# Kernel tuning notes

Hardware: AMD Instinct MI355X
Metric: run time of the kernel (lower is better)

## Reference

```python
import jax, jax.numpy as jnp
import numpy as np

N_NODES = 100000
N_EDGES = 1600000
D_FEAT = 128
HIDDEN = 128
HEADS = 4
OUT_C = HIDDEN // HEADS  # 32
N_CLASSES = 10
N_GRAPHS = 64
NEG_SLOPE = 0.2


def glorot(key, shape, fan_in, fan_out):
    s = jnp.sqrt(6.0 / (fan_in + fan_out))
    return jax.random.uniform(key, shape, minval=-s, maxval=s, dtype=jnp.float32)


def setup_inputs() -> dict:
    key = jax.random.key(0)
    ks = jax.random.split(key, 24)
    x = jax.random.normal(ks[0], (N_NODES, D_FEAT), dtype=jnp.float32)
    src = jax.random.randint(ks[1], (N_EDGES,), 0, N_NODES, dtype=jnp.int32)
    off = jax.random.randint(ks[2], (N_EDGES,), 1, N_NODES, dtype=jnp.int32)
    dst = ((src + off) % N_NODES).astype(jnp.int32)  # guarantees no self-loops
    edge_index = jnp.stack([src, dst], axis=0)
    batch = jnp.sort(jax.random.randint(ks[3], (N_NODES,), 0, N_GRAPHS, dtype=jnp.int32))
    inp = {"x": x, "edge_index": edge_index, "batch": batch}
    # GATConv layer params: W [in, H*C] (lin_l == lin_r), att_l/att_r [H, C], bias [H*C]
    ins = [D_FEAT, HIDDEN, HIDDEN]
    for i in range(3):
        k = 4 + 4 * i
        inp[f"W{i+1}"] = glorot(ks[k], (ins[i], HEADS * OUT_C), ins[i], HEADS * OUT_C)
        inp[f"al{i+1}"] = glorot(ks[k + 1], (HEADS, OUT_C), HEADS * OUT_C, 1)
        inp[f"ar{i+1}"] = glorot(ks[k + 2], (HEADS, OUT_C), HEADS * OUT_C, 1)
        inp[f"b{i+1}"] = jnp.zeros((HEADS * OUT_C,), jnp.float32)
    inp["lin1_w"] = glorot(ks[16], (HIDDEN, HIDDEN), HIDDEN, HIDDEN)
    inp["lin1_b"] = jnp.zeros((HIDDEN,), jnp.float32)
    inp["lin2_w"] = glorot(ks[17], (HIDDEN, N_CLASSES), HIDDEN, N_CLASSES)
    inp["lin2_b"] = jnp.zeros((N_CLASSES,), jnp.float32)
    return inp


def gat_layer(x, src, dst, W, att_l, att_r, bias):
    n = x.shape[0]
    H, C = att_l.shape
    xw = (x @ W).reshape(n, H, C)                       # Theta x
    al = jnp.einsum('nhc,hc->nh', xw, att_l)
    ar = jnp.einsum('nhc,hc->nh', xw, att_r)
    loop = jnp.arange(n, dtype=src.dtype)
    s = jnp.concatenate([src, loop])                    # add self-loops
    d = jnp.concatenate([dst, loop])
    logits = jax.nn.leaky_relu(al[s] + ar[d], NEG_SLOPE)  # [E+N, H]
    m = jax.ops.segment_max(logits, d, num_segments=n)    # segment softmax over dst
    e = jnp.exp(logits - m[d])
    z = jax.ops.segment_sum(e, d, num_segments=n)
    alpha = e / z[d]
    msg = xw[s] * alpha[:, :, None]                     # [E+N, H, C]
    out = jax.ops.segment_sum(msg, d, num_segments=n)   # scatter-add aggregate
    return out.reshape(n, H * C) + bias


def reference(x, edge_index, batch,
              W1, al1, ar1, b1, W2, al2, ar2, b2, W3, al3, ar3, b3,
              lin1_w, lin1_b, lin2_w, lin2_b):
    src, dst = edge_index[0], edge_index[1]
    h = jax.nn.relu(gat_layer(x, src, dst, W1, al1, ar1, b1))
    h = jax.nn.relu(gat_layer(h, src, dst, W2, al2, ar2, b2))
    h = jax.nn.relu(gat_layer(h, src, dst, W3, al3, ar3, b3))
    last = h
    # global mean pool over graphs in the batch
    s = jax.ops.segment_sum(h, batch, num_segments=N_GRAPHS)
    cnt = jax.ops.segment_sum(jnp.ones((h.shape[0],), h.dtype), batch, num_segments=N_GRAPHS)
    pooled = s / jnp.maximum(cnt, 1.0)[:, None]
    g = jax.nn.relu(pooled @ lin1_w + lin1_b)           # dropout inactive (eval)
    logits = g @ lin2_w + lin2_b
    return (jax.nn.log_softmax(logits, axis=-1), last)
```

## Files before the change

### kernel.cpp

```cpp
#include <hip/hip_runtime.h>
#include <math.h>


#define LRELU(x) ((x) > 0.f ? (x) : 0.2f*(x))
#define SH 8
#define TILE 4096
#define EPT 16
#define PSL 64

typedef __attribute__((ext_vector_type(8))) short s16x8;
typedef __attribute__((ext_vector_type(4))) float f32x4;

__device__ inline unsigned short f2bf(float f){
  unsigned u = __float_as_uint(f);
  u += 0x7fff + ((u >> 16) & 1);
  return (unsigned short)(u >> 16);
}

__global__ void k_init(int* __restrict__ bcnt, float* __restrict__ psum,
                       const float* __restrict__ W0, const float* __restrict__ W1,
                       const float* __restrict__ W2, unsigned short* __restrict__ wt3){
  int t = threadIdx.x;
  if (blockIdx.x == 0){
    bcnt[t] = 0; bcnt[256 + t] = 0;
    for (int i = t; i < 8192; i += 256) psum[i] = 0.f;
    return;
  }
  int e = ((int)blockIdx.x - 1)*256 + t;
  int layer = e >> 14, rem = e & 16383;
  int k = rem >> 7, nn = rem & 127;
  const float* Ws = layer == 0 ? W0 : (layer == 1 ? W1 : W2);
  wt3[layer*16384 + nn*128 + k] = f2bf(Ws[k*128 + nn]);
}

template<bool BF16IN>
__device__ __forceinline__ void gemm_body(
    unsigned short* Xl, unsigned short* Cl,
    const void* __restrict__ Xv, const unsigned short* __restrict__ Wtg,
    const float* __restrict__ attl, const float* __restrict__ attr,
    unsigned short* __restrict__ XW, float* __restrict__ AL, float* __restrict__ AR,
    int n, int bid, int gstride)
{
  int t = threadIdx.x;
  int lane = t & 63, w = t >> 6;
  int l15 = lane & 15, quad = lane >> 4;
  int ntiles = (n + 63) >> 6;
  int r_ = t >> 2, seg = t & 3;
  const unsigned short* Bp0 = Wtg + (w*32 + l15)*128 + quad*8;
  const unsigned short* Bp1 = Bp0 + 16*128;
  s16x8 b0r[4], b1r[4];
  #pragma unroll
  for (int ks = 0; ks < 4; ks++){
    b0r[ks] = *(const s16x8*)(Bp0 + ks*32);
    b1r[ks] = *(const s16x8*)(Bp1 + ks*32);
  }
  for (int tile = bid; tile < ntiles; tile += gstride){
    int row0 = tile << 6;
    {
      int grow = row0 + r_;
      unsigned short* dp = &Xl[r_*136 + seg*32];
      if (grow < n){
        if (BF16IN){
          const uint4* gp = (const uint4*)((const unsigned short*)Xv + (size_t)grow*128 + seg*32);
          #pragma unroll
          for (int i = 0; i < 4; i++) ((uint4*)dp)[i] = gp[i];
        } else {
          const float4* gp = (const float4*)((const float*)Xv + (size_t)grow*128 + seg*32);
          #pragma unroll
          for (int i = 0; i < 8; i++){
            float4 v = gp[i];
            ((unsigned*)dp)[i*2]   = (unsigned)f2bf(v.x) | ((unsigned)f2bf(v.y) << 16);
            ((unsigned*)dp)[i*2+1] = (unsigned)f2bf(v.z) | ((unsigned)f2bf(v.w) << 16);
          }
        }
      } else {
        #pragma unroll
        for (int i = 0; i < 4; i++) ((uint4*)dp)[i] = make_uint4(0,0,0,0);
      }
    }
    __syncthreads();
    f32x4 acc[4][2];
    #pragma unroll
    for (int rt = 0; rt < 4; rt++){ acc[rt][0] = (f32x4){0,0,0,0}; acc[rt][1] = (f32x4){0,0,0,0}; }
    #pragma unroll
    for (int ks = 0; ks < 4; ks++){
      #pragma unroll
      for (int rt = 0; rt < 4; rt++){
        s16x8 a = *(const s16x8*)&Xl[(rt*16 + l15)*136 + ks*32 + quad*8];
        acc[rt][0] = __builtin_amdgcn_mfma_f32_16x16x32_bf16(a, b0r[ks], acc[rt][0], 0, 0, 0);
        acc[rt][1] = __builtin_amdgcn_mfma_f32_16x16x32_bf16(a, b1r[ks], acc[rt][1], 0, 0, 0);
      }
    }
    #pragma unroll
    for (int rt = 0; rt < 4; rt++)
      #pragma unroll
      for (int c2 = 0; c2 < 2; c2++)
        #pragma unroll
        for (int r = 0; r < 4; r++)
          Cl[(rt*16 + quad*4 + r)*136 + w*32 + c2*16 + l15] = f2bf(acc[rt][c2][r]);
    __syncthreads();
    {
      int grow = row0 + r_;
      if (grow < n){
        const unsigned short* sp = &Cl[r_*136 + seg*32];
        uint4 uu[4];
        #pragma unroll
        for (int i = 0; i < 4; i++) uu[i] = ((const uint4*)sp)[i];
        unsigned short* gx = XW + (size_t)grow*128 + seg*32;
        #pragma unroll
        for (int i = 0; i < 4; i++) ((uint4*)gx)[i] = uu[i];
        const unsigned* up = (const unsigned*)uu;
        const float4* alp = (const float4*)(attl + seg*32);
        const float4* arp = (const float4*)(attr + seg*32);
        float pl = 0.f, pr = 0.f;
        #pragma unroll
        for (int i = 0; i < 8; i++){
          unsigned ua = up[i*2], ub = up[i*2+1];
          float x0 = __uint_as_float(ua << 16);
          float x1 = __uint_as_float(ua & 0xffff0000u);
          float x2 = __uint_as_float(ub << 16);
          float x3 = __uint_as_float(ub & 0xffff0000u);
          float4 av = alp[i];
          float4 rv = arp[i];
          pl += x0*av.x + x1*av.y + x2*av.z + x3*av.w;
          pr += x0*rv.x + x1*rv.y + x2*rv.z + x3*rv.w;
        }
        AL[grow*4 + seg] = pl;
        AR[grow*4 + seg] = pr;
      }
    }
  }
}

template<bool BF16IN>
__global__ __launch_bounds__(256) void k_gemm(
    const void* __restrict__ Xv, const unsigned short* __restrict__ Wtg,
    const float* __restrict__ attl, const float* __restrict__ attr,
    unsigned short* __restrict__ XW, float* __restrict__ AL, float* __restrict__ AR, int n)
{
  __shared__ unsigned short Xl[64*136];
  __shared__ unsigned short Cl[64*136];
  gemm_body<BF16IN>(Xl, Cl, Xv, Wtg, attl, attr, XW, AL, AR, n, blockIdx.x, gridDim.x);
}

__global__ __launch_bounds__(256) void k_fuse1(
    const int* __restrict__ dst, int* __restrict__ bcnt, int E, int nparts,
    const float* __restrict__ X, const unsigned short* __restrict__ Wtg,
    const float* __restrict__ attl, const float* __restrict__ attr,
    unsigned short* __restrict__ XW, float* __restrict__ AL, float* __restrict__ AR, int n)
{
  __shared__ unsigned short Xl[64*136];
  __shared__ unsigned short Cl[64*136];
  if ((int)blockIdx.x < nparts){
    int* lh = (int*)Xl;
    int t = threadIdx.x;
    for (int j = t; j < 512; j += 256) lh[j] = 0;
    __syncthreads();
    int base = blockIdx.x * TILE;
    int lim = min(base + TILE, E);
    for (int e = base + t; e < lim; e += 256)
      atomicAdd(&lh[dst[e] >> SH], 1);
    __syncthreads();
    for (int j = t; j < 512; j += 256){
      int v = lh[j];
      if (v) atomicAdd(&bcnt[j], v);
    }
    return;
  }
  gemm_body<false>(Xl, Cl, X, Wtg, attl, attr, XW, AL, AR, n,
                   (int)blockIdx.x - nparts, (int)gridDim.x - nparts);
}

__global__ __launch_bounds__(256) void k_bscan(const int* __restrict__ bcnt,
    int* __restrict__ bstart, int* __restrict__ bfill, int NB, int E,
    const int* __restrict__ batch, int* __restrict__ gstart, int n){
  int t = threadIdx.x;
  if (blockIdx.x == 1){
    int g = t;
    if (g > 64) return;
    int lo = 0, hi = n;
    while (lo < hi){
      int mid = (lo + hi) >> 1;
      if (batch[mid] < g) lo = mid + 1; else hi = mid;
    }
    gstart[g] = lo;
    return;
  }
  __shared__ int c[512];
  __shared__ int ps[256];
  for (int j = t; j < 512; j += 256) c[j] = (j < NB) ? bcnt[j] : 0;
  __syncthreads();
  int b0 = 2*t;
  int v0 = c[b0], v1 = c[b0+1];
  int ts = v0 + v1;
  ps[t] = ts; __syncthreads();
  for (int off = 1; off < 256; off <<= 1){
    int x = (t >= off) ? ps[t-off] : 0; __syncthreads();
    ps[t] += x; __syncthreads();
  }
  int pre = ps[t] - ts;
  if (b0   < NB){ bstart[b0]   = pre;    bfill[b0]   = pre; }
  if (b0+1 < NB){ bstart[b0+1] = pre+v0; bfill[b0+1] = pre+v0; }
  if (t == 0) bstart[NB] = E;
}

__global__ __launch_bounds__(256) void k_part(const int* __restrict__ src,
    const int* __restrict__ dst, int* __restrict__ bfill,
    int2* __restrict__ tmp, int E){
  __shared__ int2 reorder[TILE];
  __shared__ int lhist[512], lscan[512], lgbase[512];
  __shared__ int ps[256];
  int t = threadIdx.x;
  int tb = blockIdx.x * TILE;
  int tilecnt = min(TILE, E - tb);
  for (int j = t; j < 512; j += 256) lhist[j] = 0;
  __syncthreads();
  int ss[EPT], dd[EPT], rk[EPT];
  #pragma unroll
  for (int i = 0; i < EPT; i++){
    int e = tb + t + i*256;
    if (e < E){
      ss[i] = src[e]; dd[i] = dst[e];
      rk[i] = atomicAdd(&lhist[dd[i] >> SH], 1);
    }
  }
  __syncthreads();
  int b0 = 2*t;
  int v0 = lhist[b0], v1 = lhist[b0+1];
  int ts = v0 + v1;
  ps[t] = ts; __syncthreads();
  for (int off = 1; off < 256; off <<= 1){
    int x = (t >= off) ? ps[t-off] : 0; __syncthreads();
    ps[t] += x; __syncthreads();
  }
  int pre = ps[t] - ts;
  int ex0 = pre, ex1 = pre + v0;
  lscan[b0] = ex0; lscan[b0+1] = ex1;
  if (v0 > 0){ int gb = atomicAdd(&bfill[b0],   v0); lgbase[b0]   = gb - ex0; }
  if (v1 > 0){ int gb = atomicAdd(&bfill[b0+1], v1); lgbase[b0+1] = gb - ex1; }
  __syncthreads();
  #pragma unroll
  for (int i = 0; i < EPT; i++){
    int e = tb + t + i*256;
    if (e < E){
      int b = dd[i] >> SH;
      reorder[lscan[b] + rk[i]] = make_int2(ss[i], dd[i]);
    }
  }
  __syncthreads();
  for (int j = t; j < tilecnt; j += 256){
    int2 p = reorder[j];
    tmp[lgbase[p.y >> SH] + j] = p;
  }
}

__global__ __launch_bounds__(256) void k_csr(const int2* __restrict__ tmp,
    const int* __restrict__ bstart, int* __restrict__ rp, int* __restrict__ col,
    int n, int E){
  __shared__ int lcnt[256];
  __shared__ int sc[256];
  int b = blockIdx.x, t = threadIdx.x;
  int node0 = b << SH;
  int ncnt = min(256, n - node0);
  int be = bstart[b], ee = bstart[b+1];
  lcnt[t] = 0;
  __syncthreads();
  for (int e = be + t; e < ee; e += 256)
    atomicAdd(&lcnt[tmp[e].y - node0], 1);
  __syncthreads();
  int v = lcnt[t];
  sc[t] = v;
  __syncthreads();
  for (int off = 1; off < 256; off <<= 1){
    int x = (t >= off) ? sc[t-off] : 0;
    __syncthreads();
    sc[t] += x;
    __syncthreads();
  }
  int start = be + sc[t] - v;
  lcnt[t] = start;
  if (t < ncnt) rp[node0 + t] = start;
  if (t == 0 && node0 + ncnt == n) rp[n] = E;
  __syncthreads();
  for (int e = be + t; e < ee; e += 256){
    int2 p = tmp[e];
    int pos = atomicAdd(&lcnt[p.y - node0], 1);
    col[pos] = p.x;
  }
}

template<bool BF16OUT>
__global__ __launch_bounds__(256) void k_attn(
    const unsigned short* __restrict__ XW, const float* __restrict__ AL, const float* __restrict__ AR,
    const int* __restrict__ rp, const int* __restrict__ col,
    const float* __restrict__ bias, void* __restrict__ OUT, int dbase, int nmax)
{
  __shared__ int   ws[4][512];
  __shared__ float arsh[4][4][4];
  int wv = threadIdx.x >> 6;
  int lane = threadIdx.x & 63;
  int r = lane & 15, g = lane >> 4, h2 = r >> 2;
  int d0 = dbase + (blockIdx.x*4 + wv)*4;
  if (d0 >= nmax) return;
  int d = d0 + g;
  bool valid = d < nmax;
  int dc = valid ? d : nmax-1;
  int rs = rp[dc];
  int re = valid ? rp[dc+1] : rs;
  float4 ard4 = ((const float4*)AR)[dc];
  if (r == 0) *(float4*)&arsh[wv][g][0] = ard4;
  float4 ald4 = ((const float4*)AL)[dc];
  float alh = h2==0?ald4.x : h2==1?ald4.y : h2==2?ald4.z : ald4.w;
  float arh = h2==0?ard4.x : h2==1?ard4.y : h2==2?ard4.z : ard4.w;
  float tse = alh + arh;
  float eself = __expf(fmaxf(tse, 0.2f*tse));
  const uint4* XW4 = (const uint4*)XW;
  float acc[8];
  {
    uint4 v = XW4[(size_t)dc*16 + r];
    acc[0] = eself * __uint_as_float(v.x << 16);
    acc[1] = eself * __uint_as_float(v.x & 0xffff0000u);
    acc[2] = eself * __uint_as_float(v.y << 16);
    acc[3] = eself * __uint_as_float(v.y & 0xffff0000u);
    acc[4] = eself * __uint_as_float(v.z << 16);
    acc[5] = eself * __uint_as_float(v.z & 0xffff0000u);
    acc[6] = eself * __uint_as_float(v.w << 16);
    acc[7] = eself * __uint_as_float(v.w & 0xffff0000u);
  }
  int ub0 = rp[d0];
  int ubE = rp[min(d0+4, nmax)];
  int reb = valid ? re : 0x7fffffff;
  int b1 = __shfl(reb, 0, 64);
  int b2 = __shfl(reb, 16, 64);
  int b3 = __shfl(reb, 32, 64);
  int* wsw = ws[wv];
  float zacc = eself;
  for (int cb = ub0; cb < ubE; cb += 64){
    int cnt = min(64, ubE - cb);
    if (lane < cnt){
      int e = cb + lane;
      int s = col[e];
      int eg = (e >= b1) + (e >= b2) + (e >= b3);
      float4 arr = *(const float4*)&arsh[wv][eg][0];
      float4 a = ((const float4*)AL)[s];
      float t0 = a.x + arr.x, t1 = a.y + arr.y, t2 = a.z + arr.z, t3 = a.w + arr.w;
      float w0 = __expf(fmaxf(t0, 0.2f*t0));
      float w1 = __expf(fmaxf(t1, 0.2f*t1));
      float w2 = __expf(fmaxf(t2, 0.2f*t2));
      float w3 = __expf(fmaxf(t3, 0.2f*t3));
      int s4 = s << 4;
      ((int4*)&wsw[lane*8])[0] = make_int4(s4, __float_as_int(w0), s4, __float_as_int(w1));
      ((int4*)&wsw[lane*8])[1] = make_int4(s4, __float_as_int(w2), s4, __float_as_int(w3));
    }
    int jlo = max(rs - cb, 0);
    int jhi = min(re - cb, cnt);
    #pragma unroll 4
    for (int j = jlo; j < jhi; ++j){
      int2 q = *(const int2*)&wsw[j*8 + h2*2];
      float w = __int_as_float(q.y);
      uint4 u = XW4[(unsigned)(q.x + r)];
      acc[0] = fmaf(w, __uint_as_float(u.x << 16), acc[0]);
      acc[1] = fmaf(w, __uint_as_float(u.x & 0xffff0000u), acc[1]);
      acc[2] = fmaf(w, __uint_as_float(u.y << 16), acc[2]);
      acc[3] = fmaf(w, __uint_as_float(u.y & 0xffff0000u), acc[3]);
      acc[4] = fmaf(w, __uint_as_float(u.z << 16), acc[4]);
      acc[5] = fmaf(w, __uint_as_float(u.z & 0xffff0000u), acc[5]);
      acc[6] = fmaf(w, __uint_as_float(u.w << 16), acc[6]);
      acc[7] = fmaf(w, __uint_as_float(u.w & 0xffff0000u), acc[7]);
      zacc += w;
    }
  }
  float rz = 1.f / zacc;
  float4 bb0 = ((const float4*)bias)[r*2];
  float4 bb1 = ((const float4*)bias)[r*2 + 1];
  float o[8];
  o[0] = fmaf(acc[0], rz, bb0.x); o[1] = fmaf(acc[1], rz, bb0.y);
  o[2] = fmaf(acc[2], rz, bb0.z); o[3] = fmaf(acc[3], rz, bb0.w);
  o[4] = fmaf(acc[4], rz, bb1.x); o[5] = fmaf(acc[5], rz, bb1.y);
  o[6] = fmaf(acc[6], rz, bb1.z); o[7] = fmaf(acc[7], rz, bb1.w);
  #pragma unroll
  for (int i = 0; i < 8; i++) o[i] = o[i] > 0.f ? o[i] : 0.f;
  if (valid){
    if (BF16OUT){
      uint4 pk;
      pk.x = (unsigned)f2bf(o[0]) | ((unsigned)f2bf(o[1]) << 16);
      pk.y = (unsigned)f2bf(o[2]) | ((unsigned)f2bf(o[3]) << 16);
      pk.z = (unsigned)f2bf(o[4]) | ((unsigned)f2bf(o[5]) << 16);
      pk.w = (unsigned)f2bf(o[6]) | ((unsigned)f2bf(o[7]) << 16);
      ((uint4*)OUT)[(size_t)d*16 + r] = pk;
    } else {
      float4 f0; f0.x = o[0]; f0.y = o[1]; f0.z = o[2]; f0.w = o[3];
      float4 f1; f1.x = o[4]; f1.y = o[5]; f1.z = o[6]; f1.w = o[7];
      ((float4*)OUT)[(size_t)d*32 + r*2]     = f0;
      ((float4*)OUT)[(size_t)d*32 + r*2 + 1] = f1;
    }
  }
}

__global__ __launch_bounds__(128) void k_pool(const float* __restrict__ H,
                                              const int* __restrict__ gstart,
                                              float* __restrict__ psum){
  int g = blockIdx.x >> 6, slice = blockIdx.x & (PSL-1), t = threadIdx.x;
  int s0 = gstart[g], s1 = gstart[g+1];
  int cntg = s1 - s0;
  int chunk = (cntg + PSL-1) / PSL;
  int lo = s0 + slice*chunk;
  int hi = min(lo + chunk, s1);
  if (lo >= hi) return;
  float sum = 0.f;
  for (int i = lo; i < hi; i++) sum += H[(size_t)i*128 + t];
  atomicAdd(&psum[g*128 + t], sum);
}

__global__ __launch_bounds__(128) void k_mlp(const float* __restrict__ psum,
                       const int* __restrict__ gstart,
                       const float* __restrict__ w1, const float* __restrict__ b1,
                       const float* __restrict__ w2, const float* __restrict__ b2,
                       float* __restrict__ out)
{
  __shared__ float p[128];
  __shared__ float gsh[128];
  __shared__ float lg[10];
  int g = blockIdx.x, t = threadIdx.x;
  float c = fmaxf((float)(gstart[g+1] - gstart[g]), 1.f);
  p[t] = psum[g*128 + t] / c;
  __syncthreads();
  float acc = b1[t];
  for (int k = 0; k < 128; k++) acc = fmaf(p[k], w1[k*128 + t], acc);
  gsh[t] = acc > 0.f ? acc : 0.f;
  __syncthreads();
  if (t < 10){
    float a = b2[t];
    for (int k = 0; k < 128; k++) a = fmaf(gsh[k], w2[k*10 + t], a);
    lg[t] = a;
  }
  __syncthreads();
  if (t < 10){
    float mx = lg[0];
    for (int c2 = 1; c2 < 10; c2++) mx = fmaxf(mx, lg[c2]);
    float se = 0.f;
    for (int c2 = 0; c2 < 10; c2++) se += __expf(lg[c2] - mx);
    out[g*10 + t] = lg[t] - mx - logf(se);
  }
}

extern "C" void kernel_launch(void* const* d_in, const int* in_sizes, int n_in,
                              void* d_out, int out_size, void* d_ws, size_t ws_size,
                              hipStream_t stream)
{
  const float* x    = (const float*)d_in[0];
  const int* eidx   = (const int*)d_in[1];
  const int* batch  = (const int*)d_in[2];
  const float* W[3]  = {(const float*)d_in[3], (const float*)d_in[7],  (const float*)d_in[11]};
  const float* al[3] = {(const float*)d_in[4], (const float*)d_in[8],  (const float*)d_in[12]};
  const float* ar[3] = {(const float*)d_in[5], (const float*)d_in[9],  (const float*)d_in[13]};
  const float* bs[3] = {(const float*)d_in[6], (const float*)d_in[10], (const float*)d_in[14]};
  const float* l1w = (const float*)d_in[15];
  const float* l1b = (const float*)d_in[16];
  const float* l2w = (const float*)d_in[17];
  const float* l2b = (const float*)d_in[18];
  int E = in_sizes[1] / 2;
  int n = in_sizes[2];
  const int* srcp = eidx;
  const int* dstp = eidx + E;
  int NB = (n + 255) >> SH;

  char* wsp = (char*)d_ws;
  auto alloc = [&](size_t bytes){ void* p = (void*)wsp; wsp += (bytes + 255) & ~(size_t)255; return p; };
  unsigned short* xw   = (unsigned short*)alloc((size_t)n*128*2);
  unsigned short* hbuf = (unsigned short*)alloc((size_t)n*128*2);
  float* ALb  = (float*)alloc((size_t)n*4*4);
  float* ARb  = (float*)alloc((size_t)n*4*4);
  int* rp     = (int*)alloc((size_t)(n+1)*4);
  int* col    = (int*)alloc((size_t)E*4);
  int2* tmp   = (int2*)alloc((size_t)E*8);
  int* bcnt   = (int*)alloc(512*4);
  int* bstart = (int*)alloc(513*4);
  int* bfill  = (int*)alloc(512*4);
  float* psum = (float*)alloc(64*128*4);
  int* gstart = (int*)alloc(65*4);
  unsigned short* wt3 = (unsigned short*)alloc(3*16384*2);

  float* outlog = (float*)d_out;
  float* h3     = (float*)d_out + 64*10;

  int nparts = (E + TILE - 1) / TILE;

  k_init<<<193, 256, 0, stream>>>(bcnt, psum, W[0], W[1], W[2], wt3);
  k_fuse1<<<nparts + 1024, 256, 0, stream>>>(dstp, bcnt, E, nparts,
                                             x, wt3, al[0], ar[0], xw, ALb, ARb, n);
  k_bscan<<<2, 256, 0, stream>>>(bcnt, bstart, bfill, NB, E, batch, gstart, n);
  k_part <<<nparts, 256, 0, stream>>>(srcp, dstp, bfill, tmp, E);
  k_csr  <<<NB, 256, 0, stream>>>(tmp, bstart, rp, col, n, E);

  int ablk = (n + 15) / 16;
  k_attn<true><<<ablk, 256, 0, stream>>>(xw, ALb, ARb, rp, col, bs[0], hbuf, 0, n);
  k_gemm<true><<<1024, 256, 0, stream>>>(hbuf, wt3 + 16384, al[1], ar[1], xw, ALb, ARb, n);
  k_attn<true><<<ablk, 256, 0, stream>>>(xw, ALb, ARb, rp, col, bs[1], hbuf, 0, n);
  k_gemm<true><<<1024, 256, 0, stream>>>(hbuf, wt3 + 32768, al[2], ar[2], xw, ALb, ARb, n);
  k_attn<false><<<ablk, 256, 0, stream>>>(xw, ALb, ARb, rp, col, bs[2], h3, 0, n);

  k_pool<<<64*PSL, 128, 0, stream>>>(h3, gstart, psum);
  k_mlp <<<64, 128, 0, stream>>>(psum, gstart, l1w, l1b, l2w, l2b, outlog);
}
```

Measured before the change: 499.7 us.

## Split layer-1 GEMM across histogram, partition and CSR kernels

The first-layer feature GEMM was fused only into the histogram kernel. It is now split into three tile ranges that run as extra blocks inside the histogram, partition and CSR-build kernels. The aim is to hide GEMM work behind the latency-bound CSR construction phases and balance load across the three launches. Shared memory is now unioned through raw byte buffers. The GEMM blocks now use one tile per block instead of a strided persistent loop. The fixed split ratios may not match the actual per-phase slack.

```diff
diff --git a/kernel.cpp b/kernel.cpp
--- a/kernel.cpp
+++ b/kernel.cpp
@@ -39,12 +39,11 @@
     const void* __restrict__ Xv, const unsigned short* __restrict__ Wtg,
     const float* __restrict__ attl, const float* __restrict__ attr,
     unsigned short* __restrict__ XW, float* __restrict__ AL, float* __restrict__ AR,
-    int n, int bid, int gstride)
+    int n, int tlo, int thi, int bid, int gstride)
 {
   int t = threadIdx.x;
   int lane = t & 63, w = t >> 6;
   int l15 = lane & 15, quad = lane >> 4;
-  int ntiles = (n + 63) >> 6;
   int r_ = t >> 2, seg = t & 3;
   const unsigned short* Bp0 = Wtg + (w*32 + l15)*128 + quad*8;
   const unsigned short* Bp1 = Bp0 + 16*128;
@@ -54,7 +53,7 @@
     b0r[ks] = *(const s16x8*)(Bp0 + ks*32);
     b1r[ks] = *(const s16x8*)(Bp1 + ks*32);
   }
-  for (int tile = bid; tile < ntiles; tile += gstride){
+  for (int tile = tlo + bid; tile < thi; tile += gstride){
     int row0 = tile << 6;
     {
       int grow = row0 + r_;
@@ -140,14 +139,17 @@
 {
   __shared__ unsigned short Xl[64*136];
   __shared__ unsigned short Cl[64*136];
-  gemm_body<BF16IN>(Xl, Cl, Xv, Wtg, attl, attr, XW, AL, AR, n, blockIdx.x, gridDim.x);
+  int ntiles = (n + 63) >> 6;
+  gemm_body<BF16IN>(Xl, Cl, Xv, Wtg, attl, attr, XW, AL, AR, n,
+                    0, ntiles, blockIdx.x, gridDim.x);
 }
 
 __global__ __launch_bounds__(256) void k_fuse1(
     const int* __restrict__ dst, int* __restrict__ bcnt, int E, int nparts,
     const float* __restrict__ X, const unsigned short* __restrict__ Wtg,
     const float* __restrict__ attl, const float* __restrict__ attr,
-    unsigned short* __restrict__ XW, float* __restrict__ AL, float* __restrict__ AR, int n)
+    unsigned short* __restrict__ XW, float* __restrict__ AL, float* __restrict__ AR,
+    int n, int T1)
 {
   __shared__ unsigned short Xl[64*136];
   __shared__ unsigned short Cl[64*136];
@@ -168,7 +170,7 @@
     return;
   }
   gemm_body<false>(Xl, Cl, X, Wtg, attl, attr, XW, AL, AR, n,
-                   (int)blockIdx.x - nparts, (int)gridDim.x - nparts);
+                   0, T1, (int)blockIdx.x - nparts, (int)gridDim.x - nparts);
 }
 
 __global__ __launch_bounds__(256) void k_bscan(const int* __restrict__ bcnt,
@@ -204,13 +206,28 @@
   if (t == 0) bstart[NB] = E;
 }
 
-__global__ __launch_bounds__(256) void k_part(const int* __restrict__ src,
+__global__ __launch_bounds__(256) void k_part2(const int* __restrict__ src,
     const int* __restrict__ dst, int* __restrict__ bfill,
-    int2* __restrict__ tmp, int E){
-  __shared__ int2 reorder[TILE];
-  __shared__ int lhist[512], lscan[512], lgbase[512];
-  __shared__ int ps[256];
+    int2* __restrict__ tmp, int E,
+    const float* __restrict__ X, const unsigned short* __restrict__ Wtg,
+    const float* __restrict__ attl, const float* __restrict__ attr,
+    unsigned short* __restrict__ XW, float* __restrict__ AL, float* __restrict__ AR,
+    int n, int T1, int T2){
+  __shared__ __align__(16) char smem[40960];
+  int nparts = (E + TILE - 1) / TILE;
   int t = threadIdx.x;
+  if ((int)blockIdx.x >= nparts){
+    unsigned short* Xl = (unsigned short*)smem;
+    unsigned short* Cl = (unsigned short*)(smem + 17408);
+    gemm_body<false>(Xl, Cl, X, Wtg, attl, attr, XW, AL, AR, n,
+                     T1, T2, (int)blockIdx.x - nparts, (int)gridDim.x - nparts);
+    return;
+  }
+  int2* reorder = (int2*)smem;
+  int* lhist  = (int*)(smem + 32768);
+  int* lscan  = (int*)(smem + 34816);
+  int* lgbase = (int*)(smem + 36864);
+  int* ps     = (int*)(smem + 38912);
   int tb = blockIdx.x * TILE;
   int tilecnt = min(TILE, E - tb);
   for (int j = t; j < 512; j += 256) lhist[j] = 0;
@@ -254,12 +271,27 @@
   }
 }
 
-__global__ __launch_bounds__(256) void k_csr(const int2* __restrict__ tmp,
+__global__ __launch_bounds__(256) void k_csr2(const int2* __restrict__ tmp,
     const int* __restrict__ bstart, int* __restrict__ rp, int* __restrict__ col,
-    int n, int E){
-  __shared__ int lcnt[256];
-  __shared__ int sc[256];
-  int b = blockIdx.x, t = threadIdx.x;
+    int n, int E,
+    const float* __restrict__ X, const unsigned short* __restrict__ Wtg,
+    const float* __restrict__ attl, const float* __restrict__ attr,
+    unsigned short* __restrict__ XW, float* __restrict__ AL, float* __restrict__ AR,
+    int T2){
+  __shared__ __align__(16) char smem[34816];
+  int NB = (n + 255) >> SH;
+  int t = threadIdx.x;
+  if ((int)blockIdx.x >= NB){
+    unsigned short* Xl = (unsigned short*)smem;
+    unsigned short* Cl = (unsigned short*)(smem + 17408);
+    int ntiles = (n + 63) >> 6;
+    gemm_body<false>(Xl, Cl, X, Wtg, attl, attr, XW, AL, AR, n,
+                     T2, ntiles, (int)blockIdx.x - NB, (int)gridDim.x - NB);
+    return;
+  }
+  int* lcnt = (int*)smem;
+  int* sc   = (int*)(smem + 1024);
+  int b = blockIdx.x;
   int node0 = b << SH;
   int ncnt = min(256, n - node0);
   int be = bstart[b], ee = bstart[b+1];
@@ -485,13 +517,21 @@
   float* h3     = (float*)d_out + 64*10;
 
   int nparts = (E + TILE - 1) / TILE;
+  int ntiles = (n + 63) >> 6;
+  int T1 = ntiles / 6;
+  int T2 = T1 + (int)((long long)(ntiles - T1) * 54 / 100);
+  int G1 = T1 > 0 ? T1 : 1;
+  int G2 = (T2 - T1) > 0 ? (T2 - T1) : 1;
+  int G3 = (ntiles - T2) > 0 ? (ntiles - T2) : 1;
 
   k_init<<<193, 256, 0, stream>>>(bcnt, psum, W[0], W[1], W[2], wt3);
-  k_fuse1<<<nparts + 1024, 256, 0, stream>>>(dstp, bcnt, E, nparts,
-                                             x, wt3, al[0], ar[0], xw, ALb, ARb, n);
+  k_fuse1<<<nparts + G1, 256, 0, stream>>>(dstp, bcnt, E, nparts,
+                                           x, wt3, al[0], ar[0], xw, ALb, ARb, n, T1);
   k_bscan<<<2, 256, 0, stream>>>(bcnt, bstart, bfill, NB, E, batch, gstart, n);
-  k_part <<<nparts, 256, 0, stream>>>(srcp, dstp, bfill, tmp, E);
-  k_csr  <<<NB, 256, 0, stream>>>(tmp, bstart, rp, col, n, E);
+  k_part2<<<nparts + G2, 256, 0, stream>>>(srcp, dstp, bfill, tmp, E,
+                                           x, wt3, al[0], ar[0], xw, ALb, ARb, n, T1, T2);
+  k_csr2 <<<NB + G3, 256, 0, stream>>>(tmp, bstart, rp, col, n, E,
+                                       x, wt3, al[0], ar[0], xw, ALb, ARb, T2);
 
   int ablk = (n + 15) / 16;
   k_attn<true><<<ablk, 256, 0, stream>>>(xw, ALb, ARb, rp, col, bs[0], hbuf, 0, n);
```

Result: no change. 494.4 us (median of 2 runs) (-1.1%).
